# Kernel tuning notes

Hardware: AMD Instinct MI355X
Metric: run time of the kernel (lower is better)

The kernel has to match this reference:

```python
import jax, jax.numpy as jnp
import numpy as np

DIM = 1536
NH = 12
HD = DIM // NH  # 128
B = 1
F, H, W = 8, 16, 16
S = F * H * W  # 2048
EPS = 1e-6
MAX_POS = 1024


def _rmsnorm(x, g):
    # WanRMSNorm: x * rsqrt(mean(x^2, -1) + eps) * weight  (computed in fp32)
    return x * jax.lax.rsqrt(jnp.mean(x * x, axis=-1, keepdims=True) + EPS) * g


def _rope_apply(x, grid_sizes, freqs):
    # x: [B, S, NH, HD]; freqs: [1024, HD//2] angles. Full (level-0) freqs_i path.
    f, h, w = [int(v) for v in np.asarray(grid_sizes[0])]
    c = HD // 2  # 64
    s0 = c - 2 * (c // 3)  # 22 (frame freqs)
    s1 = c // 3            # 21 (height / width freqs)
    p0 = freqs[:f, :s0]
    p1 = freqs[:h, s0:s0 + s1]
    p2 = freqs[:w, s0 + s1:]
    ang = jnp.concatenate([
        jnp.broadcast_to(p0[:, None, None, :], (f, h, w, s0)),
        jnp.broadcast_to(p1[None, :, None, :], (f, h, w, s1)),
        jnp.broadcast_to(p2[None, None, :, :], (f, h, w, s1)),
    ], axis=-1).reshape(f * h * w, 1, c)  # [S, 1, c]
    cos, sin = jnp.cos(ang), jnp.sin(ang)
    xr = x[0].reshape(S, NH, c, 2)  # pairs -> complex rotation
    x0, x1 = xr[..., 0], xr[..., 1]
    out = jnp.stack([x0 * cos - x1 * sin, x0 * sin + x1 * cos], axis=-1)
    return out.reshape(S, NH, HD)[None].astype(jnp.float32)  # [1, S, NH, HD]


def setup_inputs() -> dict:
    key = jax.random.key(0)
    ks = jax.random.split(key, 8)
    sc = 0.02
    return {
        "x": jax.random.normal(ks[0], (B, S, DIM), jnp.float32),
        "freqs": jax.random.uniform(ks[1], (MAX_POS, HD // 2), jnp.float32, 0.0, 2.0 * np.pi),
        "wq": jax.random.normal(ks[2], (DIM, DIM), jnp.float32) * sc,
        "bq": jnp.zeros((DIM,), jnp.float32),
        "wk": jax.random.normal(ks[3], (DIM, DIM), jnp.float32) * sc,
        "bk": jnp.zeros((DIM,), jnp.float32),
        "wv": jax.random.normal(ks[4], (DIM, DIM), jnp.float32) * sc,
        "bv": jnp.zeros((DIM,), jnp.float32),
        "wo": jax.random.normal(ks[5], (DIM, DIM), jnp.float32) * sc,
        "bo": jnp.zeros((DIM,), jnp.float32),
        "gq": jnp.ones((DIM,), jnp.float32),
        "gk": jnp.ones((DIM,), jnp.float32),
        "seq_lens": jnp.array([S], jnp.int32),
        "grid_sizes": jnp.array([[F, H, W]], jnp.int32),
    }


def reference(x, freqs, wq, bq, wk, bk, wv, bv, wo, bo, gq, gk, seq_lens, grid_sizes):
    b, s = x.shape[:2]
    q = _rmsnorm(x @ wq.T + bq, gq).reshape(b, s, NH, HD)
    k = _rmsnorm(x @ wk.T + bk, gk).reshape(b, s, NH, HD)
    v = (x @ wv.T + bv).reshape(b, s, NH, HD)
    q = _rope_apply(q, grid_sizes, freqs)
    k = _rope_apply(k, grid_sizes, freqs)
    # flash_attention with k_lens=seq_lens, full window -> masked SDPA
    kmask = jnp.arange(s)[None, :] < seq_lens[:, None]  # [b, s]
    scores = jnp.einsum('bqnd,bknd->bnqk', q, k) / np.sqrt(HD).astype(np.float32)
    scores = jnp.where(kmask[:, None, None, :], scores, jnp.finfo(scores.dtype).min)
    attn = jax.nn.softmax(scores, axis=-1)
    out = jnp.einsum('bnqk,bknd->bqnd', attn, v).reshape(b, s, DIM)
    return out @ wo.T + bo
```

## Files before the change

### kernel.cpp

```cpp
#include <hip/hip_runtime.h>
#include <math.h>

#define DIMN 1536
#define NHEAD 12
#define HDIM 128
#define SLEN 2048
#define EPSV 1e-6f

typedef __attribute__((ext_vector_type(8))) short short8;
typedef __attribute__((ext_vector_type(4))) short short4v;
typedef __attribute__((ext_vector_type(4))) float f32x4;

typedef __attribute__((address_space(1))) const void gvoid_t;
typedef __attribute__((address_space(3))) void lvoid_t;

__device__ __forceinline__ void gload_lds16(const void* g, void* l) {
    __builtin_amdgcn_global_load_lds((gvoid_t*)g, (lvoid_t*)l, 16, 0, 0);
}

__device__ inline short to_bf16(float f) {
    union { float f; unsigned u; } v; v.f = f;
    unsigned r = (v.u + 0x7FFFu + ((v.u >> 16) & 1u)) >> 16;
    return (short)r;
}
__device__ inline float bf_to_f(short h) {
    union { unsigned u; float f; } v;
    v.u = ((unsigned)(unsigned short)h) << 16;
    return v.f;
}

__device__ __forceinline__ int swz8(int row, int c) {
    return c ^ (row & 7);
}

__global__ __launch_bounds__(256)
void cast5(const float* s0, const float* s1, const float* s2,
           const float* s3, const float* s4,
           short* d0, short* d1, short* d2, short* d3, short* d4,
           int n0, int nw)
{
    const float* s; short* d; int n;
    switch (blockIdx.y) {
        case 0: s = s0; d = d0; n = n0; break;
        case 1: s = s1; d = d1; n = nw; break;
        case 2: s = s2; d = d2; n = nw; break;
        case 3: s = s3; d = d3; n = nw; break;
        default: s = s4; d = d4; n = nw; break;
    }
    int idx = (blockIdx.x * 256 + threadIdx.x) * 8;
    if (idx >= n) return;
    float4 a = *(const float4*)(s + idx);
    float4 b = *(const float4*)(s + idx + 4);
    short8 r;
    r[0] = to_bf16(a.x); r[1] = to_bf16(a.y); r[2] = to_bf16(a.z); r[3] = to_bf16(a.w);
    r[4] = to_bf16(b.x); r[5] = to_bf16(b.y); r[6] = to_bf16(b.z); r[7] = to_bf16(b.w);
    *(short8*)(d + idx) = r;
}

__device__ __forceinline__ void gemm_mainloop(const short* __restrict__ A,
    const short* __restrict__ W, int m0, int n0, int K,
    short* As, short* Bs, f32x4 (&acc)[2][4])
{
    const int tid = threadIdx.x;
    const int wave = tid >> 6, lane = tid & 63;
    const int quad = lane >> 4, col = lane & 15;
    const int wm = wave >> 1, wn = wave & 1;
    const int sr = tid >> 3;
    const int sc = tid & 7;

    for (int kt = 0; kt < K; kt += 64) {
        __syncthreads();
        #pragma unroll
        for (int i = 0; i < 2; ++i) {
            const int row = i * 32 + sr;
            const int c = swz8(row, sc);
            gload_lds16(A + (size_t)(m0 + row) * K + kt + c * 8, As + i * 2048 + tid * 8);
        }
        #pragma unroll
        for (int i = 0; i < 4; ++i) {
            const int row = i * 32 + sr;
            const int c = swz8(row, sc);
            gload_lds16(W + (size_t)(n0 + row) * K + kt + c * 8, Bs + i * 2048 + tid * 8);
        }
        __syncthreads();

        #pragma unroll
        for (int kb = 0; kb < 2; ++kb) {
            short8 af[2], bf[4];
            #pragma unroll
            for (int mt = 0; mt < 2; ++mt) {
                const int row = wm * 32 + mt * 16 + col;
                af[mt] = *(const short8*)&As[row * 64 + swz8(row, kb * 4 + quad) * 8];
            }
            #pragma unroll
            for (int nt = 0; nt < 4; ++nt) {
                const int row = wn * 64 + nt * 16 + col;
                bf[nt] = *(const short8*)&Bs[row * 64 + swz8(row, kb * 4 + quad) * 8];
            }
            #pragma unroll
            for (int mt = 0; mt < 2; ++mt)
                #pragma unroll
                for (int nt = 0; nt < 4; ++nt)
                    acc[mt][nt] = __builtin_amdgcn_mfma_f32_16x16x32_bf16(
                        af[mt], bf[nt], acc[mt][nt], 0, 0, 0);
        }
    }
}

__global__ __launch_bounds__(256)
void gemm_qkv(const short* __restrict__ A,
              const short* __restrict__ W0, const short* __restrict__ W1,
              const short* __restrict__ W2,
              const float* __restrict__ b0, const float* __restrict__ b1,
              const float* __restrict__ b2,
              short* __restrict__ Y0, short* __restrict__ Y1,
              short* __restrict__ Vp)
{
    __shared__ __attribute__((aligned(16))) short As[64 * 64];
    __shared__ __attribute__((aligned(16))) short Bs[128 * 64];

    const int sel = blockIdx.x / (DIMN / 128);
    const int nb  = blockIdx.x % (DIMN / 128);
    const short* W    = (sel == 0) ? W0 : (sel == 1) ? W1 : W2;
    const float* bias = (sel == 0) ? b0 : (sel == 1) ? b1 : b2;

    const int tid = threadIdx.x;
    const int wave = tid >> 6, lane = tid & 63;
    const int quad = lane >> 4, col = lane & 15;
    const int wm = wave >> 1, wn = wave & 1;
    const int m0 = blockIdx.y * 64, n0 = nb * 128;

    f32x4 acc[2][4];
    #pragma unroll
    for (int i = 0; i < 2; ++i)
        #pragma unroll
        for (int j = 0; j < 4; ++j)
            #pragma unroll
            for (int r = 0; r < 4; ++r) acc[i][j][r] = 0.f;

    gemm_mainloop(A, W, m0, n0, DIMN, As, Bs, acc);

    if (sel < 2) {
        short* Y = (sel == 0) ? Y0 : Y1;
        #pragma unroll
        for (int mt = 0; mt < 2; ++mt) {
            #pragma unroll
            for (int nt = 0; nt < 4; ++nt) {
                const int n = n0 + wn * 64 + nt * 16 + col;
                const float bb = bias[n];
                #pragma unroll
                for (int r = 0; r < 4; ++r) {
                    const int m = m0 + wm * 32 + mt * 16 + quad * 4 + r;
                    Y[(size_t)m * DIMN + n] = to_bf16(acc[mt][nt][r] + bb);
                }
            }
        }
    } else {
        const int head = nb;
        const int step = blockIdx.y * 2 + wm;
        #pragma unroll
        for (int mt = 0; mt < 2; ++mt) {
            #pragma unroll
            for (int nt = 0; nt < 4; ++nt) {
                const int n = n0 + wn * 64 + nt * 16 + col;
                const float bb = bias[n];
                const int dt = wn * 4 + nt;
                const int chunk = (head * 64 + step) * 8 + dt;
                const int off = (mt * 2 + (quad >> 1)) * 128 + col * 8 + (quad & 1) * 4;
                short4v o;
                #pragma unroll
                for (int r = 0; r < 4; ++r) o[r] = to_bf16(acc[mt][nt][r] + bb);
                *(short4v*)(Vp + (size_t)chunk * 512 + off) = o;
            }
        }
    }
}

__global__ __launch_bounds__(256)
void gemm_out(const short* __restrict__ A, const short* __restrict__ W,
              const float* __restrict__ bias, float* __restrict__ Yf)
{
    __shared__ __attribute__((aligned(16))) short As[64 * 64];
    __shared__ __attribute__((aligned(16))) short Bs[128 * 64];

    const int tid = threadIdx.x;
    const int wave = tid >> 6, lane = tid & 63;
    const int quad = lane >> 4, col = lane & 15;
    const int wm = wave >> 1, wn = wave & 1;
    const int m0 = blockIdx.y * 64, n0 = blockIdx.x * 128;

    f32x4 acc[2][4];
    #pragma unroll
    for (int i = 0; i < 2; ++i)
        #pragma unroll
        for (int j = 0; j < 4; ++j)
            #pragma unroll
            for (int r = 0; r < 4; ++r) acc[i][j][r] = 0.f;

    gemm_mainloop(A, W, m0, n0, DIMN, As, Bs, acc);

    #pragma unroll
    for (int mt = 0; mt < 2; ++mt) {
        #pragma unroll
        for (int nt = 0; nt < 4; ++nt) {
            const int n = n0 + wn * 64 + nt * 16 + col;
            const float bb = bias[n];
            #pragma unroll
            for (int r = 0; r < 4; ++r) {
                const int m = m0 + wm * 32 + mt * 16 + quad * 4 + r;
                Yf[(size_t)m * DIMN + n] = acc[mt][nt][r] + bb;
            }
        }
    }
}

__global__ __launch_bounds__(256)
void rms_rope_qk(short* __restrict__ qbuf, const short* __restrict__ kbuf,
                 short* __restrict__ Kp,
                 const float* __restrict__ gq, const float* __restrict__ gk,
                 const float* __restrict__ freqs, const int* __restrict__ grid_sizes)
{
    const int s = blockIdx.x;
    const int isK = blockIdx.y;
    const int tid = threadIdx.x;
    short* qrow = qbuf + (size_t)s * DIMN;
    const short* row = isK ? (kbuf + (size_t)s * DIMN) : qrow;
    const float* g = isK ? gk : gq;

    float ss = 0.f;
    if (tid < 192) {
        short8 v = *(const short8*)(row + tid * 8);
        #pragma unroll
        for (int j = 0; j < 8; ++j) { float f = bf_to_f(v[j]); ss += f * f; }
    }
    #pragma unroll
    for (int off = 32; off; off >>= 1) ss += __shfl_down(ss, off, 64);

    __shared__ float red[4];
    __shared__ float s_scale;
    if ((tid & 63) == 0) red[tid >> 6] = ss;
    __syncthreads();
    if (tid == 0) {
        float t = red[0] + red[1] + red[2] + red[3];
        float sc = rsqrtf(t / (float)DIMN + EPSV);
        s_scale = isK ? sc : sc * 0.08838834764831845f;
    }
    __syncthreads();
    const float scale = s_scale;

    const int h = grid_sizes[1], w = grid_sizes[2];
    const int fi = s / (h * w);
    const int hi = (s / w) % h;
    const int wi = s % w;

    if (!isK) {
        for (int p = tid; p < NHEAD * 64; p += 256) {
            const int n = p >> 6;
            const int d = p & 63;
            const int idx = (d < 22) ? fi : ((d < 43) ? hi : wi);
            const float ang = freqs[idx * 64 + d];
            float sn, cs;
            __sincosf(ang, &sn, &cs);
            const int base = n * HDIM + 2 * d;
            const float v0 = bf_to_f(qrow[base]) * scale * g[base];
            const float v1 = bf_to_f(qrow[base + 1]) * scale * g[base + 1];
            qrow[base]     = to_bf16(v0 * cs - v1 * sn);
            qrow[base + 1] = to_bf16(v0 * sn + v1 * cs);
        }
    } else if (tid < 192) {
        const int n = tid >> 4;
        const int o = tid & 15;
        short8 outv;
        #pragma unroll
        for (int pp = 0; pp < 4; ++pp) {
            const int pd = o * 4 + pp;
            const int idx = (pd < 22) ? fi : ((pd < 43) ? hi : wi);
            const float ang = freqs[idx * 64 + pd];
            float sn, cs;
            __sincosf(ang, &sn, &cs);
            const int base = n * HDIM + 2 * pd;
            const float v0 = bf_to_f(row[base]) * scale * g[base];
            const float v1 = bf_to_f(row[base + 1]) * scale * g[base + 1];
            outv[pp * 2]     = to_bf16(v0 * cs - v1 * sn);
            outv[pp * 2 + 1] = to_bf16(v0 * sn + v1 * cs);
        }
        const int kb = s >> 4, colk = s & 15;
        const int kc = o >> 2, quadk = o & 3;
        const size_t addr = ((((size_t)(n * 128 + kb) * 4 + kc) * 64) + quadk * 16 + colk) * 8;
        *(short8*)(Kp + addr) = outv;
    }
}

__global__ __launch_bounds__(128)
void attn_mfma11(const short* __restrict__ Q, const short* __restrict__ Kp,
                 const short* __restrict__ Vp, short* __restrict__ O,
                 const int* __restrict__ seq_lens)
{
    __shared__ __attribute__((aligned(16))) short psw[2 * 1280];
    __shared__ __attribute__((aligned(16))) float sacc[32 * 132];
    __shared__ float sl[32];

    const int tid  = threadIdx.x;
    const int wave = tid >> 6;
    const int lane = tid & 63;
    const int quad = lane >> 4, col = lane & 15;

    const int orig = blockIdx.y * 64 + blockIdx.x;
    const int work = (orig & 7) * 96 + (orig >> 3);
    const int head = work >> 6;
    const int row0 = (work & 63) * 32;
    const int slen = seq_lens[0];

    short8 qf[2][4];
    #pragma unroll
    for (int T = 0; T < 2; ++T)
        #pragma unroll
        for (int kc = 0; kc < 4; ++kc)
            qf[T][kc] = *(const short8*)(Q + (size_t)(row0 + T * 16 + col) * DIMN
                                         + head * HDIM + kc * 32 + quad * 8);

    f32x4 oacc[2][8];
    #pragma unroll
    for (int T = 0; T < 2; ++T)
        #pragma unroll
        for (int dt = 0; dt < 8; ++dt)
            #pragma unroll
            for (int r = 0; r < 4; ++r) oacc[T][dt][r] = 0.f;
    float lsum[2][4];
    #pragma unroll
    for (int T = 0; T < 2; ++T)
        #pragma unroll
        for (int r = 0; r < 4; ++r) lsum[T][r] = 0.f;

    const short* kbase = Kp + (size_t)head * 262144 + lane * 8;
    const short* vbase = Vp + (size_t)head * 262144 + lane * 8;
    short* pswm = psw + wave * 1280;
    const int step0 = wave * 32;

    auto loadKV = [&](short8 (&kf)[8], short8 (&vf)[8], int step) {
        const short* ks = kbase + (size_t)step * 4096;
        const short* vs = vbase + (size_t)step * 4096;
        #pragma unroll
        for (int c = 0; c < 8; ++c) kf[c] = *(const short8*)(ks + c * 512);
        #pragma unroll
        for (int c = 0; c < 8; ++c) vf[c] = *(const short8*)(vs + c * 512);
    };

    auto compute = [&](short8 (&kf)[8], short8 (&vf)[8], int step) {
        f32x4 s[2][2];
        #pragma unroll
        for (int T = 0; T < 2; ++T)
            #pragma unroll
            for (int nt = 0; nt < 2; ++nt)
                #pragma unroll
                for (int r = 0; r < 4; ++r) s[T][nt][r] = 0.f;

        #pragma unroll
        for (int kc = 0; kc < 4; ++kc)
            #pragma unroll
            for (int T = 0; T < 2; ++T) {
                s[T][0] = __builtin_amdgcn_mfma_f32_16x16x32_bf16(qf[T][kc], kf[kc],     s[T][0], 0, 0, 0);
                s[T][1] = __builtin_amdgcn_mfma_f32_16x16x32_bf16(qf[T][kc], kf[4 + kc], s[T][1], 0, 0, 0);
            }

        const int kt0 = step * 32;
        #pragma unroll
        for (int T = 0; T < 2; ++T)
            #pragma unroll
            for (int nt = 0; nt < 2; ++nt) {
                const bool masked = (kt0 + nt * 16 + col >= slen);
                #pragma unroll
                for (int r = 0; r < 4; ++r) {
                    float p = masked ? 0.f : __expf(s[T][nt][r]);
                    lsum[T][r] += p;
                    pswm[T * 640 + (quad * 4 + r) * 40 + nt * 16 + col] = to_bf16(p);
                }
            }

        short8 pf0 = *(const short8*)&pswm[col * 40 + quad * 8];
        short8 pf1 = *(const short8*)&pswm[640 + col * 40 + quad * 8];

        #pragma unroll
        for (int dt = 0; dt < 8; ++dt) {
            oacc[0][dt] = __builtin_amdgcn_mfma_f32_16x16x32_bf16(pf0, vf[dt], oacc[0][dt], 0, 0, 0);
            oacc[1][dt] = __builtin_amdgcn_mfma_f32_16x16x32_bf16(pf1, vf[dt], oacc[1][dt], 0, 0, 0);
        }
    };

    short8 kA[8], vA[8], kB[8], vB[8];
    loadKV(kA, vA, step0);

    #pragma unroll 1
    for (int kt = 0; kt < 32; kt += 2) {
        loadKV(kB, vB, step0 + kt + 1);
        compute(kA, vA, step0 + kt);
        loadKV(kA, vA, step0 + kt + 2);
        compute(kB, vB, step0 + kt + 1);
    }

    #pragma unroll
    for (int T = 0; T < 2; ++T)
        #pragma unroll
        for (int r = 0; r < 4; ++r) {
            #pragma unroll
            for (int off = 8; off; off >>= 1)
                lsum[T][r] += __shfl_xor(lsum[T][r], off, 64);
        }

    if (wave == 1) {
        #pragma unroll
        for (int T = 0; T < 2; ++T) {
            #pragma unroll
            for (int dt = 0; dt < 8; ++dt)
                #pragma unroll
                for (int r = 0; r < 4; ++r)
                    sacc[(T * 16 + quad * 4 + r) * 132 + dt * 16 + col] = oacc[T][dt][r];
            if (col == 0) {
                #pragma unroll
                for (int r = 0; r < 4; ++r) sl[T * 16 + quad * 4 + r] = lsum[T][r];
            }
        }
    }
    __syncthreads();
    if (wave == 0) {
        #pragma unroll
        for (int T = 0; T < 2; ++T) {
            float inv[4];
            #pragma unroll
            for (int r = 0; r < 4; ++r)
                inv[r] = 1.0f / (lsum[T][r] + sl[T * 16 + quad * 4 + r]);
            #pragma unroll
            for (int dt = 0; dt < 8; ++dt)
                #pragma unroll
                for (int r = 0; r < 4; ++r) {
                    const float o = oacc[T][dt][r]
                                  + sacc[(T * 16 + quad * 4 + r) * 132 + dt * 16 + col];
                    O[(size_t)(row0 + T * 16 + quad * 4 + r) * DIMN
                      + head * HDIM + dt * 16 + col] = to_bf16(o * inv[r]);
                }
        }
    }
}

extern "C" void kernel_launch(void* const* d_in, const int* in_sizes, int n_in,
                              void* d_out, int out_size, void* d_ws, size_t ws_size,
                              hipStream_t stream)
{
    const float* x     = (const float*)d_in[0];
    const float* freqs = (const float*)d_in[1];
    const float* wq    = (const float*)d_in[2];
    const float* bq    = (const float*)d_in[3];
    const float* wk    = (const float*)d_in[4];
    const float* bk    = (const float*)d_in[5];
    const float* wv    = (const float*)d_in[6];
    const float* bv    = (const float*)d_in[7];
    const float* wo    = (const float*)d_in[8];
    const float* bo    = (const float*)d_in[9];
    const float* gq    = (const float*)d_in[10];
    const float* gk    = (const float*)d_in[11];
    const int* seq_lens   = (const int*)d_in[12];
    const int* grid_sizes = (const int*)d_in[13];
    float* out = (float*)d_out;

    const size_t NX = (size_t)SLEN * DIMN;
    const size_t NW = (size_t)DIMN * DIMN;
    short* xb  = (short*)d_ws;
    short* wqb = xb + NX;
    short* wkb = wqb + NW;
    short* wvb = wkb + NW;
    short* wob = wvb + NW;
    short* qb  = wob + NW;
    short* kb  = qb + NX;
    short* vp  = kb + NX;
    short* kp  = vp + NX;
    short* ob  = kp + NX;

    cast5<<<dim3(1536, 5), 256, 0, stream>>>(x, wq, wk, wv, wo,
                                             xb, wqb, wkb, wvb, wob,
                                             (int)NX, (int)NW);

    gemm_qkv<<<dim3(3 * DIMN / 128, SLEN / 64), 256, 0, stream>>>(
        xb, wqb, wkb, wvb, bq, bk, bv, qb, kb, vp);

    rms_rope_qk<<<dim3(SLEN, 2), 256, 0, stream>>>(qb, kb, kp, gq, gk, freqs, grid_sizes);

    attn_mfma11<<<dim3(64, NHEAD), 128, 0, stream>>>(qb, kp, vp, ob, seq_lens);

    gemm_out<<<dim3(DIMN / 128, SLEN / 64), 256, 0, stream>>>(ob, wob, bo, out);
}
```

Before: 236.2 us.

## Split attention KV range across four waves with tree reduction of partials

The attention kernel moves from two to four waves per block, with each wave covering a quarter of the key/value sequence instead of half. Partial output accumulators and row sums are combined through shared memory in a two-level tree reduction before normalization and store. This raises the number of concurrently active waves to hide load and MFMA latency, at the cost of more shared memory, extra barriers and the reduction traffic, plus a launch bound that may constrain registers.

```diff
diff --git a/kernel.cpp b/kernel.cpp
--- a/kernel.cpp
+++ b/kernel.cpp
@@ -291,14 +291,15 @@
     }
 }
 
-__global__ __launch_bounds__(128)
-void attn_mfma11(const short* __restrict__ Q, const short* __restrict__ Kp,
+__global__ __launch_bounds__(256, 3)
+void attn_mfma12(const short* __restrict__ Q, const short* __restrict__ Kp,
                  const short* __restrict__ Vp, short* __restrict__ O,
                  const int* __restrict__ seq_lens)
 {
-    __shared__ __attribute__((aligned(16))) short psw[2 * 1280];
-    __shared__ __attribute__((aligned(16))) float sacc[32 * 132];
-    __shared__ float sl[32];
+    __shared__ __attribute__((aligned(16))) short psw[4 * 1280];
+    __shared__ __attribute__((aligned(16))) float sacc0[32 * 132];
+    __shared__ __attribute__((aligned(16))) float sacc1[32 * 132];
+    __shared__ float sl0[32], sl1[32];
 
     const int tid  = threadIdx.x;
     const int wave = tid >> 6;
@@ -335,7 +336,7 @@
     const short* kbase = Kp + (size_t)head * 262144 + lane * 8;
     const short* vbase = Vp + (size_t)head * 262144 + lane * 8;
     short* pswm = psw + wave * 1280;
-    const int step0 = wave * 32;
+    const int step0 = wave * 16;
 
     auto loadKV = [&](short8 (&kf)[8], short8 (&vf)[8], int step) {
         const short* ks = kbase + (size_t)step * 4096;
@@ -391,7 +392,7 @@
     loadKV(kA, vA, step0);
 
     #pragma unroll 1
-    for (int kt = 0; kt < 32; kt += 2) {
+    for (int kt = 0; kt < 16; kt += 2) {
         loadKV(kB, vB, step0 + kt + 1);
         compute(kA, vA, step0 + kt);
         loadKV(kA, vA, step0 + kt + 2);
@@ -407,37 +408,54 @@
                 lsum[T][r] += __shfl_xor(lsum[T][r], off, 64);
         }
 
-    if (wave == 1) {
+    auto dump = [&](float* sa, float* sls) {
         #pragma unroll
         for (int T = 0; T < 2; ++T) {
             #pragma unroll
             for (int dt = 0; dt < 8; ++dt)
                 #pragma unroll
                 for (int r = 0; r < 4; ++r)
-                    sacc[(T * 16 + quad * 4 + r) * 132 + dt * 16 + col] = oacc[T][dt][r];
+                    sa[(T * 16 + quad * 4 + r) * 132 + dt * 16 + col] = oacc[T][dt][r];
             if (col == 0) {
                 #pragma unroll
-                for (int r = 0; r < 4; ++r) sl[T * 16 + quad * 4 + r] = lsum[T][r];
-            }
-        }
-    }
+                for (int r = 0; r < 4; ++r) sls[T * 16 + quad * 4 + r] = lsum[T][r];
+            }
+        }
+    };
+    auto accum = [&](const float* sa, const float* sls) {
+        #pragma unroll
+        for (int T = 0; T < 2; ++T) {
+            #pragma unroll
+            for (int dt = 0; dt < 8; ++dt)
+                #pragma unroll
+                for (int r = 0; r < 4; ++r)
+                    oacc[T][dt][r] += sa[(T * 16 + quad * 4 + r) * 132 + dt * 16 + col];
+            #pragma unroll
+            for (int r = 0; r < 4; ++r) lsum[T][r] += sls[T * 16 + quad * 4 + r];
+        }
+    };
+
+    if (wave == 1) dump(sacc0, sl0);
+    if (wave == 3) dump(sacc1, sl1);
+    __syncthreads();
+    if (wave == 0) accum(sacc0, sl0);
+    if (wave == 2) accum(sacc1, sl1);
+    __syncthreads();
+    if (wave == 2) dump(sacc0, sl0);
     __syncthreads();
     if (wave == 0) {
+        accum(sacc0, sl0);
         #pragma unroll
         for (int T = 0; T < 2; ++T) {
             float inv[4];
             #pragma unroll
-            for (int r = 0; r < 4; ++r)
-                inv[r] = 1.0f / (lsum[T][r] + sl[T * 16 + quad * 4 + r]);
+            for (int r = 0; r < 4; ++r) inv[r] = 1.0f / lsum[T][r];
             #pragma unroll
             for (int dt = 0; dt < 8; ++dt)
                 #pragma unroll
-                for (int r = 0; r < 4; ++r) {
-                    const float o = oacc[T][dt][r]
-                                  + sacc[(T * 16 + quad * 4 + r) * 132 + dt * 16 + col];
+                for (int r = 0; r < 4; ++r)
                     O[(size_t)(row0 + T * 16 + quad * 4 + r) * DIMN
-                      + head * HDIM + dt * 16 + col] = to_bf16(o * inv[r]);
-                }
+                      + head * HDIM + dt * 16 + col] = to_bf16(oacc[T][dt][r] * inv[r]);
         }
     }
 }
@@ -484,7 +502,7 @@
 
     rms_rope_qk<<<dim3(SLEN, 2), 256, 0, stream>>>(qb, kb, kp, gq, gk, freqs, grid_sizes);
 
-    attn_mfma11<<<dim3(64, NHEAD), 128, 0, stream>>>(qb, kp, vp, ob, seq_lens);
+    attn_mfma12<<<dim3(64, NHEAD), 256, 0, stream>>>(qb, kp, vp, ob, seq_lens);
 
     gemm_out<<<dim3(DIMN / 128, SLEN / 64), 256, 0, stream>>>(ob, wob, bo, out);
 }
```

New measurement: 290.7 us. 1.23x slower.

## Process 64 query rows per attention block with four waves sharing K/V

Applied to the files above, without the earlier changes.

The attention kernel now launches 256-thread blocks covering 64 query rows: two wave pairs each take 32 rows, and each pair splits the key range in half. A per-iteration barrier keeps the waves in lockstep, presumably so the two row-halves hit the same K/V lines in cache at the same time. The grid is halved and the work remapping is adjusted to match. Shared memory per block roughly doubles, and the extra barrier adds synchronization cost, which may reduce occupancy and the latency hiding it provides.

```diff
diff --git a/kernel.cpp b/kernel.cpp
--- a/kernel.cpp
+++ b/kernel.cpp
@@ -291,24 +291,27 @@
     }
 }
 
-__global__ __launch_bounds__(128)
-void attn_mfma11(const short* __restrict__ Q, const short* __restrict__ Kp,
+__global__ __launch_bounds__(256, 1)
+void attn_mfma14(const short* __restrict__ Q, const short* __restrict__ Kp,
                  const short* __restrict__ Vp, short* __restrict__ O,
                  const int* __restrict__ seq_lens)
 {
-    __shared__ __attribute__((aligned(16))) short psw[2 * 1280];
-    __shared__ __attribute__((aligned(16))) float sacc[32 * 132];
-    __shared__ float sl[32];
+    __shared__ __attribute__((aligned(16))) short psw[4 * 1280];
+    __shared__ __attribute__((aligned(16))) float sacc0[32 * 132];
+    __shared__ __attribute__((aligned(16))) float sacc1[32 * 132];
+    __shared__ float sl0[32], sl1[32];
 
     const int tid  = threadIdx.x;
     const int wave = tid >> 6;
     const int lane = tid & 63;
     const int quad = lane >> 4, col = lane & 15;
-
-    const int orig = blockIdx.y * 64 + blockIdx.x;
-    const int work = (orig & 7) * 96 + (orig >> 3);
-    const int head = work >> 6;
-    const int row0 = (work & 63) * 32;
+    const int rowh = wave & 1;
+    const int keyh = wave >> 1;
+
+    const int orig = blockIdx.y * 32 + blockIdx.x;
+    const int work = (orig & 7) * 48 + (orig >> 3);
+    const int head = work >> 5;
+    const int row0 = (work & 31) * 64 + rowh * 32;
     const int slen = seq_lens[0];
 
     short8 qf[2][4];
@@ -335,7 +338,7 @@
     const short* kbase = Kp + (size_t)head * 262144 + lane * 8;
     const short* vbase = Vp + (size_t)head * 262144 + lane * 8;
     short* pswm = psw + wave * 1280;
-    const int step0 = wave * 32;
+    const int step0 = keyh * 32;
 
     auto loadKV = [&](short8 (&kf)[8], short8 (&vf)[8], int step) {
         const short* ks = kbase + (size_t)step * 4096;
@@ -396,6 +399,7 @@
         compute(kA, vA, step0 + kt);
         loadKV(kA, vA, step0 + kt + 2);
         compute(kB, vB, step0 + kt + 1);
+        __builtin_amdgcn_s_barrier();
     }
 
     #pragma unroll
@@ -407,34 +411,39 @@
                 lsum[T][r] += __shfl_xor(lsum[T][r], off, 64);
         }
 
-    if (wave == 1) {
+    auto dump = [&](float* sa, float* sls) {
         #pragma unroll
         for (int T = 0; T < 2; ++T) {
             #pragma unroll
             for (int dt = 0; dt < 8; ++dt)
                 #pragma unroll
                 for (int r = 0; r < 4; ++r)
-                    sacc[(T * 16 + quad * 4 + r) * 132 + dt * 16 + col] = oacc[T][dt][r];
+                    sa[(T * 16 + quad * 4 + r) * 132 + dt * 16 + col] = oacc[T][dt][r];
             if (col == 0) {
                 #pragma unroll
-                for (int r = 0; r < 4; ++r) sl[T * 16 + quad * 4 + r] = lsum[T][r];
-            }
-        }
-    }
+                for (int r = 0; r < 4; ++r) sls[T * 16 + quad * 4 + r] = lsum[T][r];
+            }
+        }
+    };
+
+    if (wave == 2) dump(sacc0, sl0);
+    if (wave == 3) dump(sacc1, sl1);
     __syncthreads();
-    if (wave == 0) {
+    if (wave < 2) {
+        const float* sa  = (wave == 0) ? sacc0 : sacc1;
+        const float* sls = (wave == 0) ? sl0 : sl1;
         #pragma unroll
         for (int T = 0; T < 2; ++T) {
             float inv[4];
             #pragma unroll
             for (int r = 0; r < 4; ++r)
-                inv[r] = 1.0f / (lsum[T][r] + sl[T * 16 + quad * 4 + r]);
+                inv[r] = 1.0f / (lsum[T][r] + sls[T * 16 + quad * 4 + r]);
             #pragma unroll
             for (int dt = 0; dt < 8; ++dt)
                 #pragma unroll
                 for (int r = 0; r < 4; ++r) {
                     const float o = oacc[T][dt][r]
-                                  + sacc[(T * 16 + quad * 4 + r) * 132 + dt * 16 + col];
+                                  + sa[(T * 16 + quad * 4 + r) * 132 + dt * 16 + col];
                     O[(size_t)(row0 + T * 16 + quad * 4 + r) * DIMN
                       + head * HDIM + dt * 16 + col] = to_bf16(o * inv[r]);
                 }
@@ -484,7 +493,7 @@
 
     rms_rope_qk<<<dim3(SLEN, 2), 256, 0, stream>>>(qb, kb, kp, gq, gk, freqs, grid_sizes);
 
-    attn_mfma11<<<dim3(64, NHEAD), 128, 0, stream>>>(qb, kp, vp, ob, seq_lens);
+    attn_mfma14<<<dim3(32, NHEAD), 256, 0, stream>>>(qb, kp, vp, ob, seq_lens);
 
     gemm_out<<<dim3(DIMN / 128, SLEN / 64), 256, 0, stream>>>(ob, wob, bo, out);
 }
```

Result: slower. 251.4 us (+6.5%).
